# Kernel optimization log

Measured on AMD Instinct MI355X. Metric: run time of the kernel, lower is better.

The kernel has to match this reference:

```python
import jax, jax.numpy as jnp
import numpy as np

B, T, DIM = 256, 2048, 64
THETA, MU, SIGMA = 0.1, 0.0, 1.0


def setup_inputs() -> dict:
    key = jax.random.key(0)
    k1, k2 = jax.random.split(key)
    # strictly increasing positive times, shape [B, T, 1]
    dt = jax.random.uniform(k1, (B, T, 1), minval=1e-3, maxval=1e-2, dtype=jnp.float32)
    ts = jnp.cumsum(dt, axis=1)
    # standard normal reparameterization noise for Normal(0, delta_ts).rsample()
    noise = jax.random.normal(k2, (B, T, DIM), dtype=jnp.float32)
    return {"ts": ts, "noise": noise}


def reference(ts, noise):
    h = DIM // 2  # slice_index
    # t_prev: 0 at step 0, ts[:, :-1] afterwards
    t_prev = jnp.concatenate([jnp.zeros_like(ts[:, :1]), ts[:, :-1]], axis=1)  # [B,T,1]
    # Brownian-increment std: sqrt(t_k - t_{k-1})  (sqrt(t_0) at k=0)
    db = jnp.sqrt(ts - t_prev)  # [B,T,1]
    # OU-increment std: sqrt(exp(2*theta*t_k) - exp(2*theta*t_{k-1}))  (exp(0)=1 at k=0)
    dou = jnp.sqrt(jnp.exp(2.0 * THETA * ts) - jnp.exp(2.0 * THETA * t_prev))  # [B,T,1]
    bt = ts.shape[:-1]
    delta = jnp.concatenate([jnp.broadcast_to(db, bt + (h,)),
                             jnp.broadcast_to(dou, bt + (h,))], axis=-1)  # [B,T,DIM]
    invalid = delta <= 0.0
    delta = jnp.where(invalid, delta + 1e-4, delta)
    # rsample = 0 + delta * eps; zero out invalid entries
    r = jnp.where(invalid, 0.0, delta * noise)
    # per-half scaling
    scale = jnp.concatenate([jnp.full((h,), np.sqrt(SIGMA), dtype=r.dtype),
                             jnp.full((h,), SIGMA / np.sqrt(2.0 * THETA), dtype=r.dtype)])
    r = r * scale
    out = jnp.cumsum(r, axis=-2)  # scan along time
    # OU mean-reversion transform on second half
    e = jnp.exp(-THETA * ts)  # [B,T,1]
    ou = e * out[..., h:] + MU * (1.0 - e)
    # normalize=True branch
    bm = out[..., :h] / (SIGMA * jnp.sqrt(ts) + 1e-8)
    ou = ou / (SIGMA * jnp.sqrt((1.0 - jnp.exp(-2.0 * THETA * ts)) / (2.0 * THETA)) + 1e-8)
    return jnp.concatenate([bm, ou], axis=-1)  # [B,T,DIM]
```

## Files before the change

kernel.cpp:

```cpp
#include <hip/hip_runtime.h>
#include <hip/hip_bf16.h>
#include <cstddef>

#define B_   256
#define T_   2048
#define DIM_ 64
#define OU_SCALE 2.2360679774997896f

__global__ void coef_kernel(const float* __restrict__ ts,
                            float4* __restrict__ coef) {
    int i = blockIdx.x * blockDim.x + threadIdx.x;
    if (i >= B_ * T_) return;
    int t = i & (T_ - 1);
    float tk = ts[i];
    float tp = (t == 0) ? 0.0f : ts[i - 1];
    float dt = tk - tp;

    float db = sqrtf(dt);
    float e2p = expf(0.2f * tp);
    float dou = sqrtf(e2p * expm1f(0.2f * dt));

    float cb = (db  <= 0.0f) ? 0.0f : db;
    float co = (dou <= 0.0f) ? 0.0f : dou * OU_SCALE;

    float fb = 1.0f / (sqrtf(tk) + 1e-8f);
    float em = expf(-0.1f * tk);
    float one_m = -expm1f(-0.2f * tk);
    float fo = em / (sqrtf(one_m * 5.0f) + 1e-8f);

    coef[i] = make_float4(cb, co, fb, fo);
}

#define UNROLL 32

__global__ __launch_bounds__(64) void scan_kernel(
        const float4* __restrict__ coef,
        const float* __restrict__ noise,
        float* __restrict__ out) {
    const int b = blockIdx.x;
    const int d = threadIdx.x;
    const bool ou_half = (d >= (DIM_ / 2));

    const float*  np_ = noise + (size_t)b * T_ * DIM_ + d;
    float*        op  = out   + (size_t)b * T_ * DIM_ + d;
    const float4* cp  = coef  + (size_t)b * T_;

    float acc = 0.0f;

    for (int t0 = 0; t0 < T_; t0 += UNROLL) {
        float  v[UNROLL];
        float4 c[UNROLL];
#pragma unroll
        for (int u = 0; u < UNROLL; ++u)
            v[u] = np_[(size_t)(t0 + u) * DIM_];
#pragma unroll
        for (int u = 0; u < UNROLL; ++u)
            c[u] = cp[t0 + u];
#pragma unroll
        for (int u = 0; u < UNROLL; ++u) {
            float delta = ou_half ? c[u].y : c[u].x;
            float f     = ou_half ? c[u].w : c[u].z;
            acc = fmaf(delta, v[u], acc);
            op[(size_t)(t0 + u) * DIM_] = acc * f;
        }
    }
}

extern "C" void kernel_launch(void* const* d_in, const int* in_sizes, int n_in,
                              void* d_out, int out_size, void* d_ws, size_t ws_size,
                              hipStream_t stream) {
    const float* ts    = (const float*)d_in[0];
    const float* noise = (const float*)d_in[1];
    float* out = (float*)d_out;
    float4* coef = (float4*)d_ws;

    int n = B_ * T_;
    coef_kernel<<<(n + 255) / 256, 256, 0, stream>>>(ts, coef);
    scan_kernel<<<B_, DIM_, 0, stream>>>(coef, noise, out);
}
```

Before: 300.9 us.

## Split time scan into chunked reduce-then-scan across more blocks

Replaces the single sequential scan per batch (256 blocks of 64 threads) with a two-pass chunked scan. Time is split into 16 chunks. A first kernel computes per-chunk partial sums, and a second kernel adds the preceding partials and rescans each chunk to write the output. This raises the block count to 4096 to fill the GPU and hide latency. The cost is reading the noise and coefficients twice plus an extra launch.

Measured after the change: 273.1 us. -9.2%, faster.

```diff
diff --git a/kernel.cpp b/kernel.cpp
--- a/kernel.cpp
+++ b/kernel.cpp
@@ -5,6 +5,8 @@
 #define B_   256
 #define T_   2048
 #define DIM_ 64
+#define C_   16
+#define L_   (T_ / C_)
 #define OU_SCALE 2.2360679774997896f
 
 __global__ void coef_kernel(const float* __restrict__ ts,
@@ -31,35 +33,67 @@
     coef[i] = make_float4(cb, co, fb, fo);
 }
 
-#define UNROLL 32
+#define UN 16
 
-__global__ __launch_bounds__(64) void scan_kernel(
+__global__ __launch_bounds__(64) void partial_kernel(
         const float4* __restrict__ coef,
         const float* __restrict__ noise,
-        float* __restrict__ out) {
-    const int b = blockIdx.x;
+        float* __restrict__ partials) {
+    const int b = blockIdx.x >> 4;
+    const int c = blockIdx.x & (C_ - 1);
     const int d = threadIdx.x;
-    const bool ou_half = (d >= (DIM_ / 2));
+    const bool ou = (d >= DIM_ / 2);
 
-    const float*  np_ = noise + (size_t)b * T_ * DIM_ + d;
-    float*        op  = out   + (size_t)b * T_ * DIM_ + d;
-    const float4* cp  = coef  + (size_t)b * T_;
+    const float*  np_ = noise + ((size_t)b * T_ + (size_t)c * L_) * DIM_ + d;
+    const float4* cp  = coef + (size_t)b * T_ + c * L_;
 
     float acc = 0.0f;
+    for (int t0 = 0; t0 < L_; t0 += UN) {
+        float  v[UN];
+        float4 cc[UN];
+#pragma unroll
+        for (int u = 0; u < UN; ++u) v[u] = np_[(size_t)(t0 + u) * DIM_];
+#pragma unroll
+        for (int u = 0; u < UN; ++u) cc[u] = cp[t0 + u];
+#pragma unroll
+        for (int u = 0; u < UN; ++u) {
+            float delta = ou ? cc[u].y : cc[u].x;
+            acc = fmaf(delta, v[u], acc);
+        }
+    }
+    partials[(size_t)blockIdx.x * DIM_ + d] = acc;
+}
 
-    for (int t0 = 0; t0 < T_; t0 += UNROLL) {
-        float  v[UNROLL];
-        float4 c[UNROLL];
+__global__ __launch_bounds__(64) void final_kernel(
+        const float4* __restrict__ coef,
+        const float* __restrict__ noise,
+        const float* __restrict__ partials,
+        float* __restrict__ out) {
+    const int b = blockIdx.x >> 4;
+    const int c = blockIdx.x & (C_ - 1);
+    const int d = threadIdx.x;
+    const bool ou = (d >= DIM_ / 2);
+
+    const float*  np_ = noise + ((size_t)b * T_ + (size_t)c * L_) * DIM_ + d;
+    const float4* cp  = coef + (size_t)b * T_ + c * L_;
+    float*        op  = out + ((size_t)b * T_ + (size_t)c * L_) * DIM_ + d;
+    const float*  pp  = partials + (size_t)(b << 4) * DIM_ + d;
+
+    float base = 0.0f;
+    for (int k = 0; k < c; ++k) base += pp[(size_t)k * DIM_];
+
+    float acc = base;
+    for (int t0 = 0; t0 < L_; t0 += UN) {
+        float  v[UN];
+        float4 cc[UN];
 #pragma unroll
-        for (int u = 0; u < UNROLL; ++u)
-            v[u] = np_[(size_t)(t0 + u) * DIM_];
+        for (int u = 0; u < UN; ++u) v[u] = np_[(size_t)(t0 + u) * DIM_];
 #pragma unroll
-        for (int u = 0; u < UNROLL; ++u)
-            c[u] = cp[t0 + u];
+        for (int u = 0; u < UN; ++u) cc[u] = cp[t0 + u];
 #pragma unroll
-        for (int u = 0; u < UNROLL; ++u) {
-            float delta = ou_half ? c[u].y : c[u].x;
-            float f     = ou_half ? c[u].w : c[u].z;
+        for (int u = 0; u < UN; ++u) {
+            float delta = ou ? cc[u].y : cc[u].x;
+            float f     = ou ? cc[u].w : cc[u].z;
             acc = fmaf(delta, v[u], acc);
             op[(size_t)(t0 + u) * DIM_] = acc * f;
         }
@@ -72,9 +106,12 @@
     const float* ts    = (const float*)d_in[0];
     const float* noise = (const float*)d_in[1];
     float* out = (float*)d_out;
-    float4* coef = (float4*)d_ws;
+
+    float4* coef     = (float4*)d_ws;
+    float*  partials = (float*)((char*)d_ws + (size_t)B_ * T_ * 16);
 
     int n = B_ * T_;
     coef_kernel<<<(n + 255) / 256, 256, 0, stream>>>(ts, coef);
-    scan_kernel<<<B_, DIM_, 0, stream>>>(coef, noise, out);
+    partial_kernel<<<B_ * C_, DIM_, 0, stream>>>(coef, noise, partials);
+    final_kernel<<<B_ * C_, DIM_, 0, stream>>>(coef, noise, partials, out);
 }
```

## Fuse coefficient and scan kernels; split time scan across 16 wavefronts with chunk partials

Applied to the files above, without the earlier changes.

Merges the coefficient kernel into the scan kernel, keeping per-timestep coefficients in shared memory instead of a workspace buffer. Each block now runs 16 wavefronts that each own a time chunk: a first pass computes chunk partial sums with vectorized float4 loads, and a second pass rescans each chunk seeded by the prefix of earlier partials. This raises parallelism from 64 threads per batch row to 1024 and removes the serial dependency across all 2048 steps. The cost is reading the noise twice and an extra synchronization round.

After: 253.4 us. 1.19x faster.

```diff
diff --git a/kernel.cpp b/kernel.cpp
--- a/kernel.cpp
+++ b/kernel.cpp
@@ -1,68 +1,89 @@
 #include <hip/hip_runtime.h>
-#include <hip/hip_bf16.h>
 #include <cstddef>
 
 #define B_   256
 #define T_   2048
 #define DIM_ 64
+#define NW   16
+#define CH   (T_ / NW)
 #define OU_SCALE 2.2360679774997896f
 
-__global__ void coef_kernel(const float* __restrict__ ts,
-                            float4* __restrict__ coef) {
-    int i = blockIdx.x * blockDim.x + threadIdx.x;
-    if (i >= B_ * T_) return;
-    int t = i & (T_ - 1);
-    float tk = ts[i];
-    float tp = (t == 0) ? 0.0f : ts[i - 1];
-    float dt = tk - tp;
+__global__ __launch_bounds__(1024) void fused_kernel(
+        const float* __restrict__ ts,
+        const float* __restrict__ noise,
+        float* __restrict__ out)
+{
+    __shared__ float4 cofs[T_];
+    __shared__ float4 par4[NW * 16];
 
-    float db = sqrtf(dt);
-    float e2p = expf(0.2f * tp);
-    float dou = sqrtf(e2p * expm1f(0.2f * dt));
+    const int b   = blockIdx.x;
+    const int tid = threadIdx.x;
+    const int w   = tid >> 6;
+    const int l   = tid & 63;
 
-    float cb = (db  <= 0.0f) ? 0.0f : db;
-    float co = (dou <= 0.0f) ? 0.0f : dou * OU_SCALE;
+    const float* tsb = ts + (size_t)b * T_;
+    for (int t = tid; t < T_; t += 1024) {
+        float tk = tsb[t];
+        float tp = (t == 0) ? 0.0f : tsb[t - 1];
+        float dt = tk - tp;
 
-    float fb = 1.0f / (sqrtf(tk) + 1e-8f);
-    float em = expf(-0.1f * tk);
-    float one_m = -expm1f(-0.2f * tk);
-    float fo = em / (sqrtf(one_m * 5.0f) + 1e-8f);
+        float db  = sqrtf(dt);
+        float dou = sqrtf(expf(0.2f * tp) * expm1f(0.2f * dt));
 
-    coef[i] = make_float4(cb, co, fb, fo);
-}
+        float cb = (db  <= 0.0f) ? 0.0f : db;
+        float co = (dou <= 0.0f) ? 0.0f : dou * OU_SCALE;
 
-#define UNROLL 32
+        float fb = 1.0f / (sqrtf(tk) + 1e-8f);
+        float em = expf(-0.1f * tk);
+        float fo = em / (sqrtf(-expm1f(-0.2f * tk) * 5.0f) + 1e-8f);
 
-__global__ __launch_bounds__(64) void scan_kernel(
-        const float4* __restrict__ coef,
-        const float* __restrict__ noise,
-        float* __restrict__ out) {
-    const int b = blockIdx.x;
-    const int d = threadIdx.x;
-    const bool ou_half = (d >= (DIM_ / 2));
+        cofs[t] = make_float4(cb, co, fb, fo);
+    }
+    __syncthreads();
 
-    const float*  np_ = noise + (size_t)b * T_ * DIM_ + d;
-    float*        op  = out   + (size_t)b * T_ * DIM_ + d;
-    const float4* cp  = coef  + (size_t)b * T_;
+    const size_t rowbase = (size_t)b * T_ * DIM_;
 
+    if (w != NW - 1) {
+        const int  g   = l >> 4;
+        const int  dq  = (l & 15) << 2;
+        const bool ouA = (dq >= DIM_ / 2);
+        const int  tb  = w * CH;
+        float4 a = make_float4(0.f, 0.f, 0.f, 0.f);
+#pragma unroll 8
+        for (int i = 0; i < CH / 4; ++i) {
+            const int t = tb + (i << 2) + g;
+            const float4 v = *(const float4*)(noise + rowbase + (size_t)t * DIM_ + dq);
+            const float4 c = cofs[t];
+            const float delta = ouA ? c.y : c.x;
+            a.x = fmaf(delta, v.x, a.x);
+            a.y = fmaf(delta, v.y, a.y);
+            a.z = fmaf(delta, v.z, a.z);
+            a.w = fmaf(delta, v.w, a.w);
+        }
+        a.x += __shfl_xor(a.x, 16); a.y += __shfl_xor(a.y, 16);
+        a.z += __shfl_xor(a.z, 16); a.w += __shfl_xor(a.w, 16);
+        a.x += __shfl_xor(a.x, 32); a.y += __shfl_xor(a.y, 32);
+        a.z += __shfl_xor(a.z, 32); a.w += __shfl_xor(a.w, 32);
+        if (l < 16) par4[w * 16 + l] = a;
+    }
+    __syncthreads();
+
+    const float* parf = (const float*)par4;
     float acc = 0.0f;
+    for (int k = 0; k < w; ++k) acc += parf[k * DIM_ + l];
 
-    for (int t0 = 0; t0 < T_; t0 += UNROLL) {
-        float  v[UNROLL];
-        float4 c[UNROLL];
-#pragma unroll
-        for (int u = 0; u < UNROLL; ++u)
-            v[u] = np_[(size_t)(t0 + u) * DIM_];
-#pragma unroll
-        for (int u = 0; u < UNROLL; ++u)
-            c[u] = cp[t0 + u];
-#pragma unroll
-        for (int u = 0; u < UNROLL; ++u) {
-            float delta = ou_half ? c[u].y : c[u].x;
-            float f     = ou_half ? c[u].w : c[u].z;
-            acc = fmaf(delta, v[u], acc);
-            op[(size_t)(t0 + u) * DIM_] = acc * f;
-        }
+    const bool ou  = (l >= DIM_ / 2);
+    const float* np_ = noise + rowbase + l;
+    float*       op  = out   + rowbase + l;
+    const int tb = w * CH;
+#pragma unroll 8
+    for (int t = tb; t < tb + CH; ++t) {
+        float v = np_[(size_t)t * DIM_];
+        float4 c = cofs[t];
+        float delta = ou ? c.y : c.x;
+        float f     = ou ? c.w : c.z;
+        acc = fmaf(delta, v, acc);
+        op[(size_t)t * DIM_] = acc * f;
     }
 }
 
@@ -72,9 +93,7 @@
     const float* ts    = (const float*)d_in[0];
     const float* noise = (const float*)d_in[1];
     float* out = (float*)d_out;
-    float4* coef = (float4*)d_ws;
+    (void)d_ws; (void)ws_size;
 
-    int n = B_ * T_;
-    coef_kernel<<<(n + 255) / 256, 256, 0, stream>>>(ts, coef);
-    scan_kernel<<<B_, DIM_, 0, stream>>>(coef, noise, out);
+    fused_kernel<<<B_, NW * 64, 0, stream>>>(ts, noise, out);
 }
```
